# Optimization experiments

Measured on AMD Instinct MI355X. Metric: run time of the kernel, lower is better.

The kernel has to match this reference:

```python
import jax, jax.numpy as jnp
import numpy as np

N_NODES = 50000
N_EDGES = 1_600_000
HID = 64
BN_EPS = 1e-5


def setup_inputs() -> dict:
    key = jax.random.key(0)
    ks = jax.random.split(key, 16)
    x = jax.random.normal(ks[0], (N_NODES, 1), dtype=jnp.float32)
    edge_index = jax.random.randint(ks[1], (2, N_EDGES), 0, N_NODES, dtype=jnp.int32)
    s = 1.0 / np.sqrt(HID)
    # layer 1: 1 -> 64 -> 64
    w1a = jax.random.normal(ks[2], (1, HID), dtype=jnp.float32)
    b1a = jnp.zeros((HID,), jnp.float32)
    w2a = jax.random.normal(ks[3], (HID, HID), dtype=jnp.float32) * s
    b2a = jnp.zeros((HID,), jnp.float32)
    # layers 2-4 stacked: 64 -> 64 -> 64
    w1s = jax.random.normal(ks[4], (3, HID, HID), dtype=jnp.float32) * s
    b1s = jnp.zeros((3, HID), jnp.float32)
    w2s = jax.random.normal(ks[5], (3, HID, HID), dtype=jnp.float32) * s
    b2s = jnp.zeros((3, HID), jnp.float32)
    eps = jnp.zeros((4,), jnp.float32)  # train_eps=True, init 0
    gammas = jnp.ones((4, HID), jnp.float32)
    betas = jnp.zeros((4, HID), jnp.float32)
    fc_w = jax.random.normal(ks[6], (HID, 1), dtype=jnp.float32) * s
    fc_b = jnp.zeros((1,), jnp.float32)
    return {"x": x, "edge_index": edge_index, "w1a": w1a, "b1a": b1a,
            "w2a": w2a, "b2a": b2a, "w1s": w1s, "b1s": b1s, "w2s": w2s,
            "b2s": b2s, "eps": eps, "gammas": gammas, "betas": betas,
            "fc_w": fc_w, "fc_b": fc_b}


def _gin(h, src, dst, e, w1, b1, w2, b2):
    # sum_{j in N(i)} h_j  (messages from src, aggregated at dst)
    agg = jax.ops.segment_sum(h[src], dst, num_segments=N_NODES)
    z = (1.0 + e) * h + agg
    return jax.nn.relu(z @ w1 + b1) @ w2 + b2


def _bn(h, g, b):
    # BatchNorm1d, training mode: biased batch statistics over nodes
    mu = jnp.mean(h, axis=0)
    var = jnp.mean((h - mu) ** 2, axis=0)
    return (h - mu) * jax.lax.rsqrt(var + BN_EPS) * g + b


def reference(x, edge_index, w1a, b1a, w2a, b2a, w1s, b1s, w2s, b2s,
              eps, gammas, betas, fc_w, fc_b):
    src, dst = edge_index[0], edge_index[1]
    h = _bn(jax.nn.relu(_gin(x, src, dst, eps[0], w1a, b1a, w2a, b2a)),
            gammas[0], betas[0])
    for i in range(3):
        h = _bn(jax.nn.relu(_gin(h, src, dst, eps[i + 1],
                                 w1s[i], b1s[i], w2s[i], b2s[i])),
                gammas[i + 1], betas[i + 1])
    return h @ fc_w + fc_b
```

## Files before the change

kernel.cpp:

```cpp
#include <hip/hip_runtime.h>
#include <hip/hip_fp16.h>

#define HID 64
#define BN_EPS 1e-5f
#define WINSH 8
#define WINSZ 256
#define B1 256
#define PIT 72

typedef short bf16x8 __attribute__((ext_vector_type(8)));
typedef float f32x4 __attribute__((ext_vector_type(4)));

__device__ __forceinline__ unsigned short f2b(float f) {
    unsigned int u = __float_as_uint(f);
    u = (u + 0x7FFF + ((u >> 16) & 1)) >> 16;
    return (unsigned short)u;
}
__device__ __forceinline__ float b2f(unsigned short h) {
    return __uint_as_float(((unsigned int)h) << 16);
}
__device__ __forceinline__ f32x4 mfma_bf16(bf16x8 a, bf16x8 b, f32x4 c) {
    return __builtin_amdgcn_mfma_f32_16x16x32_bf16(a, b, c, 0, 0, 0);
}

__global__ __launch_bounds__(256) void prep_kernel(const float* __restrict__ w2a,
                                                   const float* __restrict__ w1s,
                                                   const float* __restrict__ w2s,
                                                   unsigned short* __restrict__ whi,
                                                   unsigned short* __restrict__ wlo,
                                                   float* __restrict__ stats,
                                                   const int* __restrict__ dst,
                                                   int* __restrict__ cnt,
                                                   int E, int nw, int chunk) {
    int blk = blockIdx.x, tid = threadIdx.x;
    if (blk < 7) {
        const float* srcm = (blk == 0) ? w2a : (blk <= 3 ? w1s + (size_t)(blk - 1) * 4096
                                                         : w2s + (size_t)(blk - 4) * 4096);
        unsigned short* dh = whi + (size_t)blk * 4096;
        unsigned short* dl = wlo + (size_t)blk * 4096;
        for (int idx = tid; idx < 4096; idx += 256) {
            int j = idx & 7;
            int lane = (idx >> 3) & 63;
            int ntkh = idx >> 9;
            int nt = ntkh >> 1, kh = ntkh & 1;
            int nc = nt * 16 + (lane & 15);
            int k = kh * 32 + (lane >> 4) * 8 + j;
            float v = srcm[k * 64 + nc];
            unsigned short h = f2b(v);
            dh[idx] = h;
            dl[idx] = f2b(v - b2f(h));
        }
    } else if (blk == 7) {
        stats[tid] = 0.f;
        stats[tid + 256] = 0.f;
    } else {
        __shared__ int c[256];
        int b = blk - 8;
        c[tid] = 0;
        __syncthreads();
        int lo = b * chunk;
        int hi = lo + chunk; if (hi > E) hi = E;
        if ((((size_t)(dst + lo)) & 15) == 0) {
            int n4 = (hi - lo) >> 2;
            const int4* d4p = (const int4*)(dst + lo);
            for (int g = tid; g < n4; g += 256) {
                int4 d4 = d4p[g];
                atomicAdd(&c[d4.x >> WINSH], 1);
                atomicAdd(&c[d4.y >> WINSH], 1);
                atomicAdd(&c[d4.z >> WINSH], 1);
                atomicAdd(&c[d4.w >> WINSH], 1);
            }
            for (int e = lo + (n4 << 2) + tid; e < hi; e += 256)
                atomicAdd(&c[dst[e] >> WINSH], 1);
        } else {
            for (int e = lo + tid; e < hi; e += 256) atomicAdd(&c[dst[e] >> WINSH], 1);
        }
        __syncthreads();
        if (tid < nw) cnt[tid * B1 + b] = c[tid];
    }
}

__global__ __launch_bounds__(256) void scan_a_kernel(const int* __restrict__ in,
                                                     int* __restrict__ partial,
                                                     int* __restrict__ blocksum, int n) {
    __shared__ int sums[256];
    int tid = threadIdx.x;
    int i = blockIdx.x * 256 + tid;
    int v = (i < n) ? in[i] : 0;
    sums[tid] = v;
    __syncthreads();
    for (int off = 1; off < 256; off <<= 1) {
        int t = (tid >= off) ? sums[tid - off] : 0;
        __syncthreads();
        sums[tid] += t;
        __syncthreads();
    }
    if (i < n) partial[i] = sums[tid] - v;
    if (tid == 255) blocksum[blockIdx.x] = sums[255];
}

__global__ __launch_bounds__(256) void p3_bucket_kernel(const int* __restrict__ src,
                                                        const int* __restrict__ dst,
                                                        const int* __restrict__ cpart,
                                                        const int* __restrict__ bsum,
                                                        int* __restrict__ ebuf,
                                                        int E, int nw, int chunk, int nbs2) {
    __shared__ int cur[256];
    __shared__ int sc[256];
    int tid = threadIdx.x, b = blockIdx.x;
    int v = (tid < nbs2) ? bsum[tid] : 0;
    sc[tid] = v;
    __syncthreads();
    for (int off = 1; off < 256; off <<= 1) {
        int t = (tid >= off) ? sc[tid - off] : 0;
        __syncthreads();
        sc[tid] += t;
        __syncthreads();
    }
    int excl = sc[tid] - v;
    if (tid < nw) cur[tid] = cpart[tid * B1 + b] + excl;
    __syncthreads();
    int lo = b * chunk;
    int hi = lo + chunk; if (hi > E) hi = E;
    if (((((size_t)(dst + lo)) | ((size_t)(src + lo))) & 15) == 0) {
        int n4 = (hi - lo) >> 2;
        const int4* d4p = (const int4*)(dst + lo);
        const int4* s4p = (const int4*)(src + lo);
        for (int g = tid; g < n4; g += 256) {
            int4 d4 = d4p[g];
            int4 s4 = s4p[g];
            int p0 = atomicAdd(&cur[d4.x >> WINSH], 1);
            ebuf[p0] = s4.x | ((d4.x & (WINSZ - 1)) << 24);
            int p1 = atomicAdd(&cur[d4.y >> WINSH], 1);
            ebuf[p1] = s4.y | ((d4.y & (WINSZ - 1)) << 24);
            int p2 = atomicAdd(&cur[d4.z >> WINSH], 1);
            ebuf[p2] = s4.z | ((d4.z & (WINSZ - 1)) << 24);
            int p3 = atomicAdd(&cur[d4.w >> WINSH], 1);
            ebuf[p3] = s4.w | ((d4.w & (WINSZ - 1)) << 24);
        }
        for (int e = lo + (n4 << 2) + tid; e < hi; e += 256) {
            int d = dst[e];
            int pos = atomicAdd(&cur[d >> WINSH], 1);
            ebuf[pos] = src[e] | ((d & (WINSZ - 1)) << 24);
        }
    } else {
        for (int e = lo + tid; e < hi; e += 256) {
            int d = dst[e];
            int pos = atomicAdd(&cur[d >> WINSH], 1);
            ebuf[pos] = src[e] | ((d & (WINSZ - 1)) << 24);
        }
    }
}

__global__ __launch_bounds__(256) void p4_fine_kernel(const int* __restrict__ ebuf,
                                                      const int* __restrict__ cpart,
                                                      const int* __restrict__ bsum,
                                                      int* __restrict__ csr_src,
                                                      int* __restrict__ rowptr,
                                                      int* __restrict__ deg,
                                                      int E, int n, int nw, int nbs2) {
    __shared__ int fcnt[256];
    __shared__ int foff[256];
    int tid = threadIdx.x, w = blockIdx.x;
    int bv = (tid < nbs2) ? bsum[tid] : 0;
    foff[tid] = bv;
    __syncthreads();
    for (int off = 1; off < 256; off <<= 1) {
        int t = (tid >= off) ? foff[tid - off] : 0;
        __syncthreads();
        foff[tid] += t;
        __syncthreads();
    }
    int excl = foff[tid] - bv;
    __syncthreads();
    foff[tid] = excl;
    __syncthreads();
    int lo = cpart[w * B1] + foff[w];
    int hi = (w + 1 < nw) ? cpart[(w + 1) * B1] + foff[w + 1] : E;
    __syncthreads();
    fcnt[tid] = 0;
    __syncthreads();
    for (int e = lo + tid; e < hi; e += 256) atomicAdd(&fcnt[(unsigned)ebuf[e] >> 24], 1);
    __syncthreads();
    int v = fcnt[tid];
    foff[tid] = v;
    __syncthreads();
    for (int off = 1; off < 256; off <<= 1) {
        int t = (tid >= off) ? foff[tid - off] : 0;
        __syncthreads();
        foff[tid] += t;
        __syncthreads();
    }
    int myoff = lo + foff[tid] - v;
    int node = w * WINSZ + tid;
    if (node < n) { rowptr[node] = myoff; deg[node] = v; }
    __syncthreads();
    fcnt[tid] = myoff;
    __syncthreads();
    for (int e = lo + tid; e < hi; e += 256) {
        int p = ebuf[e];
        int pos = atomicAdd(&fcnt[(unsigned)p >> 24], 1);
        csr_src[pos] = p & 0xFFFFFF;
    }
}

__global__ __launch_bounds__(256) void gather1_kernel(const float* __restrict__ x,
                                                      const int* __restrict__ rowptr,
                                                      const int* __restrict__ deg,
                                                      const int* __restrict__ csr_src,
                                                      const float* __restrict__ eps,
                                                      float* __restrict__ zscalar, int n) {
    int node = blockIdx.x * 4 + (threadIdx.x >> 6);
    int lane = threadIdx.x & 63;
    if (node >= n) return;
    int start = __builtin_amdgcn_readfirstlane(rowptr[node]);
    int cnt   = __builtin_amdgcn_readfirstlane(deg[node]);
    float a = 0.f;
    for (int i = lane; i < cnt; i += 64) a += x[csr_src[start + i]];
    for (int off = 32; off > 0; off >>= 1) a += __shfl_xor(a, off);
    if (lane == 0) zscalar[node] = (1.0f + eps[0]) * x[node] + a;
}

__global__ __launch_bounds__(256) void gatherz_kernel(const __half* __restrict__ hh16,
                                                      const float* __restrict__ stats_prev,
                                                      const float* __restrict__ gamma_prev,
                                                      const float* __restrict__ beta_prev,
                                                      const int* __restrict__ rowptr,
                                                      const int* __restrict__ deg,
                                                      const int* __restrict__ csr_src,
                                                      const float* __restrict__ eps,
                                                      int layer,
                                                      __half* __restrict__ zh16, int n) {
    int lane = threadIdx.x & 63;
    int half = lane >> 5;
    int fp = lane & 31;
    int node = blockIdx.x * 4 + (threadIdx.x >> 6);

    float inv_n = 1.0f / (float)n;
    float2 sm = ((const float2*)stats_prev)[fp];
    float2 sq = ((const float2*)(stats_prev + 64))[fp];
    float2 gm = ((const float2*)gamma_prev)[fp];
    float2 bt = ((const float2*)beta_prev)[fp];
    float mux = sm.x * inv_n, muy = sm.y * inv_n;
    float scx = gm.x * rsqrtf(sq.x * inv_n - mux * mux + BN_EPS);
    float scy = gm.y * rsqrtf(sq.y * inv_n - muy * muy + BN_EPS);
    float shx = bt.x - mux * scx;
    float shy = bt.y - muy * scy;

    if (node >= n) return;
    int start = __builtin_amdgcn_readfirstlane(rowptr[node]);
    int cnt   = __builtin_amdgcn_readfirstlane(deg[node]);

    const __half2* hh2 = (const __half2*)hh16;
    float ax0 = 0.f, ay0 = 0.f, ax1 = 0.f, ay1 = 0.f;
    float ax2 = 0.f, ay2 = 0.f, ax3 = 0.f, ay3 = 0.f;
    float ax4 = 0.f, ay4 = 0.f, ax5 = 0.f, ay5 = 0.f;
    float ax6 = 0.f, ay6 = 0.f, ax7 = 0.f, ay7 = 0.f;
    int e = 0;
    for (; e + 16 <= cnt; e += 16) {
        int b0  = csr_src[start + e + 0];
        int b1  = csr_src[start + e + 1];
        int b2  = csr_src[start + e + 2];
        int b3  = csr_src[start + e + 3];
        int b4  = csr_src[start + e + 4];
        int b5  = csr_src[start + e + 5];
        int b6  = csr_src[start + e + 6];
        int b7  = csr_src[start + e + 7];
        int b8  = csr_src[start + e + 8];
        int b9  = csr_src[start + e + 9];
        int b10 = csr_src[start + e + 10];
        int b11 = csr_src[start + e + 11];
        int b12 = csr_src[start + e + 12];
        int b13 = csr_src[start + e + 13];
        int b14 = csr_src[start + e + 14];
        int b15 = csr_src[start + e + 15];
        int r0 = half ? b1  : b0;
        int r1 = half ? b3  : b2;
        int r2 = half ? b5  : b4;
        int r3 = half ? b7  : b6;
        int r4 = half ? b9  : b8;
        int r5 = half ? b11 : b10;
        int r6 = half ? b13 : b12;
        int r7 = half ? b15 : b14;
        float2 v0 = __half22float2(hh2[(size_t)r0 * 32 + fp]);
        float2 v1 = __half22float2(hh2[(size_t)r1 * 32 + fp]);
        float2 v2 = __half22float2(hh2[(size_t)r2 * 32 + fp]);
        float2 v3 = __half22float2(hh2[(size_t)r3 * 32 + fp]);
        float2 v4 = __half22float2(hh2[(size_t)r4 * 32 + fp]);
        float2 v5 = __half22float2(hh2[(size_t)r5 * 32 + fp]);
        float2 v6 = __half22float2(hh2[(size_t)r6 * 32 + fp]);
        float2 v7 = __half22float2(hh2[(size_t)r7 * 32 + fp]);
        ax0 += v0.x; ay0 += v0.y;
        ax1 += v1.x; ay1 += v1.y;
        ax2 += v2.x; ay2 += v2.y;
        ax3 += v3.x; ay3 += v3.y;
        ax4 += v4.x; ay4 += v4.y;
        ax5 += v5.x; ay5 += v5.y;
        ax6 += v6.x; ay6 += v6.y;
        ax7 += v7.x; ay7 += v7.y;
    }
    for (; e + 8 <= cnt; e += 8) {
        int s0 = csr_src[start + e + 0];
        int s1 = csr_src[start + e + 1];
        int s2 = csr_src[start + e + 2];
        int s3 = csr_src[start + e + 3];
        int s4 = csr_src[start + e + 4];
        int s5 = csr_src[start + e + 5];
        int s6 = csr_src[start + e + 6];
        int s7 = csr_src[start + e + 7];
        int r0 = half ? s1 : s0;
        int r1 = half ? s3 : s2;
        int r2 = half ? s5 : s4;
        int r3 = half ? s7 : s6;
        float2 v0 = __half22float2(hh2[(size_t)r0 * 32 + fp]);
        float2 v1 = __half22float2(hh2[(size_t)r1 * 32 + fp]);
        float2 v2 = __half22float2(hh2[(size_t)r2 * 32 + fp]);
        float2 v3 = __half22float2(hh2[(size_t)r3 * 32 + fp]);
        ax0 += v0.x; ay0 += v0.y;
        ax1 += v1.x; ay1 += v1.y;
        ax2 += v2.x; ay2 += v2.y;
        ax3 += v3.x; ay3 += v3.y;
    }
    for (; e < cnt; e += 2) {
        int idx = e + half;
        if (idx < cnt) {
            int s = csr_src[start + idx];
            float2 v = __half22float2(hh2[(size_t)s * 32 + fp]);
            ax0 += v.x; ay0 += v.y;
        }
    }
    float sx = ((ax0 + ax1) + (ax2 + ax3)) + ((ax4 + ax5) + (ax6 + ax7));
    float sy = ((ay0 + ay1) + (ay2 + ay3)) + ((ay4 + ay5) + (ay6 + ay7));
    sx += __shfl_xor(sx, 32);
    sy += __shfl_xor(sy, 32);

    float ep = 1.0f + eps[layer];
    float2 self = __half22float2(hh2[(size_t)node * 32 + fp]);
    float zx = fmaf(scx, fmaf(ep, self.x, sx), shx * (ep + (float)cnt));
    float zy = fmaf(scy, fmaf(ep, self.y, sy), shy * (ep + (float)cnt));
    if (half == 0) {
        ((__half2*)zh16)[(size_t)node * 32 + fp] = __floats2half2_rn(zx, zy);
    }
}

__global__ __launch_bounds__(256) void mlp_kernel(const __half* __restrict__ zh16,
                                                  const float* __restrict__ zscalar,
                                                  const float* __restrict__ w1a,
                                                  const float* __restrict__ b1a,
                                                  const unsigned short* __restrict__ w1h,
                                                  const unsigned short* __restrict__ w1l,
                                                  const float* __restrict__ b1v,
                                                  const unsigned short* __restrict__ w2h,
                                                  const unsigned short* __restrict__ w2l,
                                                  const float* __restrict__ b2v,
                                                  float* __restrict__ hpre,
                                                  __half* __restrict__ hh16,
                                                  float* __restrict__ stats,
                                                  int n, int mode,
                                                  int write_hpre, int write_hh) {
    __shared__ __align__(16) unsigned short Ah[64 * PIT];
    __shared__ __align__(16) unsigned short Al[64 * PIT];
    __shared__ float ssum[64], ssq[64];

    int tid = threadIdx.x;
    int base = blockIdx.x * 64;

    if (mode) {
        const unsigned int* z32 = (const unsigned int*)zh16;
        for (int i = tid; i < 2048; i += 256) {
            int nn = i >> 5, c = i & 31;
            unsigned int u = z32[(size_t)(base + nn) * 32 + c];
            __half2 hv = *(__half2*)&u;
            float vx = __half2float(hv.x);
            float vy = __half2float(hv.y);
            unsigned short hx = f2b(vx);
            unsigned short hy = f2b(vy);
            Ah[nn * PIT + 2 * c]     = hx;
            Ah[nn * PIT + 2 * c + 1] = hy;
            Al[nn * PIT + 2 * c]     = f2b(vx - b2f(hx));
            Al[nn * PIT + 2 * c + 1] = f2b(vy - b2f(hy));
        }
    } else {
        for (int i = tid; i < 4096; i += 256) {
            int nn = i >> 6, k = i & 63;
            float zv = zscalar[base + nn];
            float v = fmaxf(fmaf(zv, w1a[k], b1a[k]), 0.f);
            unsigned short h = f2b(v);
            Ah[nn * PIT + k] = h;
            Al[nn * PIT + k] = f2b(v - b2f(h));
        }
    }
    if (tid < 64) { ssum[tid] = 0.f; ssq[tid] = 0.f; }
    __syncthreads();

    int l = tid & 63;
    int m = l & 15;
    int q = l >> 4;
    int m0 = (tid >> 6) * 16;

    const bf16x8* a0h = (const bf16x8*)&Ah[(m0 + m) * PIT + q * 8];
    const bf16x8* a1h = (const bf16x8*)&Ah[(m0 + m) * PIT + 32 + q * 8];
    const bf16x8* a0l = (const bf16x8*)&Al[(m0 + m) * PIT + q * 8];
    const bf16x8* a1l = (const bf16x8*)&Al[(m0 + m) * PIT + 32 + q * 8];

    if (mode) {
        bf16x8 xa0h = *a0h, xa1h = *a1h, xa0l = *a0l, xa1l = *a1l;
        f32x4 acc[4];
#pragma unroll
        for (int nt = 0; nt < 4; ++nt) {
            size_t fo0 = ((size_t)(nt * 2 + 0) * 64 + l) * 8;
            size_t fo1 = ((size_t)(nt * 2 + 1) * 64 + l) * 8;
            bf16x8 b0h = *(const bf16x8*)(w1h + fo0);
            bf16x8 b1h_ = *(const bf16x8*)(w1h + fo1);
            bf16x8 b0l = *(const bf16x8*)(w1l + fo0);
            bf16x8 b1l_ = *(const bf16x8*)(w1l + fo1);
            f32x4 c = {0.f, 0.f, 0.f, 0.f};
            c = mfma_bf16(xa0h, b0h, c);
            c = mfma_bf16(xa0h, b0l, c);
            c = mfma_bf16(xa0l, b0h, c);
            c = mfma_bf16(xa1h, b1h_, c);
            c = mfma_bf16(xa1h, b1l_, c);
            c = mfma_bf16(xa1l, b1h_, c);
            acc[nt] = c;
        }
#pragma unroll
        for (int nt = 0; nt < 4; ++nt) {
            int col = nt * 16 + m;
            float bv = b1v[col];
#pragma unroll
            for (int r = 0; r < 4; ++r) {
                int row = m0 + q * 4 + r;
                float T = fmaxf(acc[nt][r] + bv, 0.f);
                unsigned short h = f2b(T);
                Ah[row * PIT + col] = h;
                Al[row * PIT + col] = f2b(T - b2f(h));
            }
        }
    }
    __syncthreads();

    {
        bf16x8 xa0h = *a0h, xa1h = *a1h, xa0l = *a0l, xa1l = *a1l;
        f32x4 acc[4];
#pragma unroll
        for (int nt = 0; nt < 4; ++nt) {
            size_t fo0 = ((size_t)(nt * 2 + 0) * 64 + l) * 8;
            size_t fo1 = ((size_t)(nt * 2 + 1) * 64 + l) * 8;
            bf16x8 b0h = *(const bf16x8*)(w2h + fo0);
            bf16x8 b1h_ = *(const bf16x8*)(w2h + fo1);
            bf16x8 b0l = *(const bf16x8*)(w2l + fo0);
            bf16x8 b1l_ = *(const bf16x8*)(w2l + fo1);
            f32x4 c = {0.f, 0.f, 0.f, 0.f};
            c = mfma_bf16(xa0h, b0h, c);
            c = mfma_bf16(xa0h, b0l, c);
            c = mfma_bf16(xa0l, b0h, c);
            c = mfma_bf16(xa1h, b1h_, c);
            c = mfma_bf16(xa1h, b1l_, c);
            c = mfma_bf16(xa1l, b1h_, c);
            acc[nt] = c;
        }
#pragma unroll
        for (int nt = 0; nt < 4; ++nt) {
            int col = nt * 16 + m;
            float bv = b2v[col];
            float cs = 0.f, cq = 0.f;
#pragma unroll
            for (int r = 0; r < 4; ++r) {
                int node = base + m0 + q * 4 + r;
                float h = fmaxf(acc[nt][r] + bv, 0.f);
                if (node < n) {
                    if (write_hpre) hpre[(size_t)node * HID + col] = h;
                    if (write_hh) hh16[(size_t)node * HID + col] = __float2half(h);
                    cs += h;
                    cq = fmaf(h, h, cq);
                }
            }
            cs += __shfl_xor(cs, 16); cs += __shfl_xor(cs, 32);
            cq += __shfl_xor(cq, 16); cq += __shfl_xor(cq, 32);
            if (q == 0) {
                atomicAdd(&ssum[col], cs);
                atomicAdd(&ssq[col], cq);
            }
        }
    }
    __syncthreads();
    if (tid < 64) {
        atomicAdd(&stats[tid], ssum[tid]);
        atomicAdd(&stats[64 + tid], ssq[tid]);
    }
}

__global__ __launch_bounds__(256) void final_kernel(const float* __restrict__ hpre,
                                                    const float* __restrict__ stats,
                                                    const float* __restrict__ gamma,
                                                    const float* __restrict__ beta,
                                                    const float* __restrict__ fcw,
                                                    const float* __restrict__ fcb,
                                                    float* __restrict__ out, int n) {
    int wave = threadIdx.x >> 6;
    int lane = threadIdx.x & 63;
    int node = blockIdx.x * 4 + wave;
    if (node < n) {
        float inv_n = 1.0f / (float)n;
        float mu = stats[lane] * inv_n;
        float var = stats[64 + lane] * inv_n - mu * mu;
        float inv = rsqrtf(var + BN_EPS);
        float sc = gamma[lane] * inv;
        float sh = beta[lane] - mu * sc;
        float v = hpre[(size_t)node * HID + lane];
        float t = fmaf(v, sc, sh) * fcw[lane];
        for (int off = 32; off > 0; off >>= 1) t += __shfl_xor(t, off);
        if (lane == 0) out[node] = t + fcb[0];
    }
}

extern "C" void kernel_launch(void* const* d_in, const int* in_sizes, int n_in,
                              void* d_out, int out_size, void* d_ws, size_t ws_size,
                              hipStream_t stream) {
    const float* x      = (const float*)d_in[0];
    const int*   ei     = (const int*)d_in[1];
    const float* w1a    = (const float*)d_in[2];
    const float* b1a    = (const float*)d_in[3];
    const float* w2a    = (const float*)d_in[4];
    const float* b2a    = (const float*)d_in[5];
    const float* w1s    = (const float*)d_in[6];
    const float* b1s    = (const float*)d_in[7];
    const float* w2s    = (const float*)d_in[8];
    const float* b2s    = (const float*)d_in[9];
    const float* eps    = (const float*)d_in[10];
    const float* gammas = (const float*)d_in[11];
    const float* betas  = (const float*)d_in[12];
    const float* fcw    = (const float*)d_in[13];
    const float* fcb    = (const float*)d_in[14];
    float* out = (float*)d_out;

    int n = in_sizes[0];
    int E = in_sizes[1] / 2;
    int npad = ((n + 63) / 64) * 64;
    int nblk = npad / 64;

    int nw = (n + WINSZ - 1) >> WINSH;
    int NWB = nw * B1;
    int chunk = (((E + B1 - 1) / B1) + 3) & ~3;
    int nbs2 = (NWB + 255) / 256;

    const int* src = ei;
    const int* dst = ei + E;

    char* p = (char*)d_ws;
    float* csrtmp  = (float*)p; p += (size_t)npad * HID * 4;
    float* hpre    = (float*)p; p += (size_t)npad * HID * 4;
    __half* hh16   = (__half*)p; p += (size_t)npad * HID * 2;
    __half* zh16   = (__half*)p; p += (size_t)npad * HID * 2;
    float* zscalar = (float*)p; p += (size_t)npad * 4;
    float* stats   = (float*)p; p += 4 * 128 * 4;
    unsigned short* whi = (unsigned short*)p; p += 7 * 4096 * 2;
    unsigned short* wlo = (unsigned short*)p; p += 7 * 4096 * 2;
    int* deg     = (int*)p; p += (size_t)n * 4;
    int* rowptr  = (int*)p; p += (size_t)n * 4;
    int* csr_src = (int*)p; p += (size_t)E * 4;

    int* ebuf     = (int*)csrtmp;
    int* cnt      = ebuf + E;
    int* cpart    = cnt + NWB;
    int* bsum     = cpart + NWB;

    prep_kernel<<<8 + B1, 256, 0, stream>>>(w2a, w1s, w2s, whi, wlo, stats,
                                            dst, cnt, E, nw, chunk);
    scan_a_kernel<<<nbs2, 256, 0, stream>>>(cnt, cpart, bsum, NWB);
    p3_bucket_kernel<<<B1, 256, 0, stream>>>(src, dst, cpart, bsum, ebuf, E, nw, chunk, nbs2);
    p4_fine_kernel<<<nw, 256, 0, stream>>>(ebuf, cpart, bsum, csr_src, rowptr, deg,
                                           E, n, nw, nbs2);

    gather1_kernel<<<(n + 3) / 4, 256, 0, stream>>>(x, rowptr, deg, csr_src, eps, zscalar, n);
    mlp_kernel<<<nblk, 256, 0, stream>>>(zh16, zscalar, w1a, b1a,
                                         whi, wlo, b1a ,
                                         whi , wlo, b2a,
                                         hpre, hh16, stats, n, 0,
                                         0, 1);

    for (int l = 1; l <= 3; ++l) {
        gatherz_kernel<<<(n + 3) / 4, 256, 0, stream>>>(hh16,
                                                        stats + (l - 1) * 128,
                                                        gammas + (l - 1) * HID,
                                                        betas + (l - 1) * HID,
                                                        rowptr, deg, csr_src, eps, l, zh16, n);
        mlp_kernel<<<nblk, 256, 0, stream>>>(zh16, zscalar, w1a, b1a,
                                             whi + (size_t)l * 4096,
                                             wlo + (size_t)l * 4096,
                                             b1s + (size_t)(l - 1) * HID,
                                             whi + (size_t)(3 + l) * 4096,
                                             wlo + (size_t)(3 + l) * 4096,
                                             b2s + (size_t)(l - 1) * HID,
                                             hpre, hh16, stats + l * 128,
                                             n, 1,
                                             (l == 3) ? 1 : 0,
                                             (l < 3) ? 1 : 0);
    }
    final_kernel<<<(n + 3) / 4, 256, 0, stream>>>(hpre, stats + 3 * 128,
                                                  gammas + 3 * HID, betas + 3 * HID,
                                                  fcw, fcb, out, n);
}
```

Baseline: 369.8 us.

## Build CSR with global atomic counting sort and fuse layer-1 gather into scatter

Replaces the two-level windowed bucket sort (shared-memory window counts, bucket scatter, per-window fine sort) with a per-node degree count using global atomics, a scan to rowptr, and a scatter that claims CSR slots via global atomic cursors. The scatter also accumulates x[src] into xsum with float atomics, so the first-layer gather kernel is removed and the MLP computes z directly. This removes kernel launches and the intermediate edge buffer pass, at the cost of heavy contended global atomics over 1.6M edges. Neighbor order within a row and the float sum order become nondeterministic.

```diff
diff --git a/kernel.cpp b/kernel.cpp
--- a/kernel.cpp
+++ b/kernel.cpp
@@ -3,8 +3,6 @@
 
 #define HID 64
 #define BN_EPS 1e-5f
-#define WINSH 8
-#define WINSZ 256
 #define B1 256
 #define PIT 72
 
@@ -21,6 +19,17 @@
 }
 __device__ __forceinline__ f32x4 mfma_bf16(bf16x8 a, bf16x8 b, f32x4 c) {
     return __builtin_amdgcn_mfma_f32_16x16x32_bf16(a, b, c, 0, 0, 0);
+}
+
+__global__ __launch_bounds__(256) void zero_kernel(int* __restrict__ deg,
+                                                   float* __restrict__ xsum,
+                                                   float* __restrict__ stats, int n) {
+    int i = blockIdx.x * 256 + threadIdx.x;
+    if (i < n) { deg[i] = 0; xsum[i] = 0.f; }
+    if (blockIdx.x == 0) {
+        stats[threadIdx.x] = 0.f;
+        stats[threadIdx.x + 256] = 0.f;
+    }
 }
 
 __global__ __launch_bounds__(256) void prep_kernel(const float* __restrict__ w2a,
@@ -28,10 +37,9 @@
                                                    const float* __restrict__ w2s,
                                                    unsigned short* __restrict__ whi,
                                                    unsigned short* __restrict__ wlo,
-                                                   float* __restrict__ stats,
                                                    const int* __restrict__ dst,
-                                                   int* __restrict__ cnt,
-                                                   int E, int nw, int chunk) {
+                                                   int* __restrict__ deg,
+                                                   int E, int chunk) {
     int blk = blockIdx.x, tid = threadIdx.x;
     if (blk < 7) {
         const float* srcm = (blk == 0) ? w2a : (blk <= 3 ? w1s + (size_t)(blk - 1) * 4096
@@ -50,14 +58,8 @@
             dh[idx] = h;
             dl[idx] = f2b(v - b2f(h));
         }
-    } else if (blk == 7) {
-        stats[tid] = 0.f;
-        stats[tid + 256] = 0.f;
     } else {
-        __shared__ int c[256];
-        int b = blk - 8;
-        c[tid] = 0;
-        __syncthreads();
+        int b = blk - 7;
         int lo = b * chunk;
         int hi = lo + chunk; if (hi > E) hi = E;
         if ((((size_t)(dst + lo)) & 15) == 0) {
@@ -65,18 +67,16 @@
             const int4* d4p = (const int4*)(dst + lo);
             for (int g = tid; g < n4; g += 256) {
                 int4 d4 = d4p[g];
-                atomicAdd(&c[d4.x >> WINSH], 1);
-                atomicAdd(&c[d4.y >> WINSH], 1);
-                atomicAdd(&c[d4.z >> WINSH], 1);
-                atomicAdd(&c[d4.w >> WINSH], 1);
+                atomicAdd(&deg[d4.x], 1);
+                atomicAdd(&deg[d4.y], 1);
+                atomicAdd(&deg[d4.z], 1);
+                atomicAdd(&deg[d4.w], 1);
             }
             for (int e = lo + (n4 << 2) + tid; e < hi; e += 256)
-                atomicAdd(&c[dst[e] >> WINSH], 1);
+                atomicAdd(&deg[dst[e]], 1);
         } else {
-            for (int e = lo + tid; e < hi; e += 256) atomicAdd(&c[dst[e] >> WINSH], 1);
-        }
-        __syncthreads();
-        if (tid < nw) cnt[tid * B1 + b] = c[tid];
+            for (int e = lo + tid; e < hi; e += 256) atomicAdd(&deg[dst[e]], 1);
+        }
     }
 }
 
@@ -99,16 +99,15 @@
     if (tid == 255) blocksum[blockIdx.x] = sums[255];
 }
 
-__global__ __launch_bounds__(256) void p3_bucket_kernel(const int* __restrict__ src,
-                                                        const int* __restrict__ dst,
-                                                        const int* __restrict__ cpart,
-                                                        const int* __restrict__ bsum,
-                                                        int* __restrict__ ebuf,
-                                                        int E, int nw, int chunk, int nbs2) {
-    __shared__ int cur[256];
+__global__ __launch_bounds__(256) void finalize_kernel(const int* __restrict__ partial,
+                                                       const int* __restrict__ bsum,
+                                                       int* __restrict__ rowptr,
+                                                       int* __restrict__ cursor,
+                                                       int n, int nbs) {
     __shared__ int sc[256];
-    int tid = threadIdx.x, b = blockIdx.x;
-    int v = (tid < nbs2) ? bsum[tid] : 0;
+    __shared__ int myoff;
+    int tid = threadIdx.x;
+    int v = (tid < nbs) ? bsum[tid] : 0;
     sc[tid] = v;
     __syncthreads();
     for (int off = 1; off < 256; off <<= 1) {
@@ -117,9 +116,24 @@
         sc[tid] += t;
         __syncthreads();
     }
-    int excl = sc[tid] - v;
-    if (tid < nw) cur[tid] = cpart[tid * B1 + b] + excl;
+    if (tid == blockIdx.x) myoff = sc[tid] - v;
     __syncthreads();
+    int i = blockIdx.x * 256 + tid;
+    if (i < n) {
+        int r = partial[i] + myoff;
+        rowptr[i] = r;
+        cursor[i] = r;
+    }
+}
+
+__global__ __launch_bounds__(256) void scatter_kernel(const int* __restrict__ src,
+                                                      const int* __restrict__ dst,
+                                                      const float* __restrict__ x,
+                                                      int* __restrict__ cursor,
+                                                      int* __restrict__ csr_src,
+                                                      float* __restrict__ xsum,
+                                                      int E, int chunk) {
+    int tid = threadIdx.x, b = blockIdx.x;
     int lo = b * chunk;
     int hi = lo + chunk; if (hi > E) hi = E;
     if (((((size_t)(dst + lo)) | ((size_t)(src + lo))) & 15) == 0) {
@@ -129,96 +143,33 @@
         for (int g = tid; g < n4; g += 256) {
             int4 d4 = d4p[g];
             int4 s4 = s4p[g];
-            int p0 = atomicAdd(&cur[d4.x >> WINSH], 1);
-            ebuf[p0] = s4.x | ((d4.x & (WINSZ - 1)) << 24);
-            int p1 = atomicAdd(&cur[d4.y >> WINSH], 1);
-            ebuf[p1] = s4.y | ((d4.y & (WINSZ - 1)) << 24);
-            int p2 = atomicAdd(&cur[d4.z >> WINSH], 1);
-            ebuf[p2] = s4.z | ((d4.z & (WINSZ - 1)) << 24);
-            int p3 = atomicAdd(&cur[d4.w >> WINSH], 1);
-            ebuf[p3] = s4.w | ((d4.w & (WINSZ - 1)) << 24);
+            int p0 = atomicAdd(&cursor[d4.x], 1);
+            csr_src[p0] = s4.x;
+            atomicAdd(&xsum[d4.x], x[s4.x]);
+            int p1 = atomicAdd(&cursor[d4.y], 1);
+            csr_src[p1] = s4.y;
+            atomicAdd(&xsum[d4.y], x[s4.y]);
+            int p2 = atomicAdd(&cursor[d4.z], 1);
+            csr_src[p2] = s4.z;
+            atomicAdd(&xsum[d4.z], x[s4.z]);
+            int p3 = atomicAdd(&cursor[d4.w], 1);
+            csr_src[p3] = s4.w;
+            atomicAdd(&xsum[d4.w], x[s4.w]);
         }
         for (int e = lo + (n4 << 2) + tid; e < hi; e += 256) {
-            int d = dst[e];
-            int pos = atomicAdd(&cur[d >> WINSH], 1);
-            ebuf[pos] = src[e] | ((d & (WINSZ - 1)) << 24);
+            int d = dst[e], s = src[e];
+            int pos = atomicAdd(&cursor[d], 1);
+            csr_src[pos] = s;
+            atomicAdd(&xsum[d], x[s]);
         }
     } else {
         for (int e = lo + tid; e < hi; e += 256) {
-            int d = dst[e];
-            int pos = atomicAdd(&cur[d >> WINSH], 1);
-            ebuf[pos] = src[e] | ((d & (WINSZ - 1)) << 24);
-        }
-    }
-}
-
-__global__ __launch_bounds__(256) void p4_fine_kernel(const int* __restrict__ ebuf,
-                                                      const int* __restrict__ cpart,
-                                                      const int* __restrict__ bsum,
-                                                      int* __restrict__ csr_src,
-                                                      int* __restrict__ rowptr,
-                                                      int* __restrict__ deg,
-                                                      int E, int n, int nw, int nbs2) {
-    __shared__ int fcnt[256];
-    __shared__ int foff[256];
-    int tid = threadIdx.x, w = blockIdx.x;
-    int bv = (tid < nbs2) ? bsum[tid] : 0;
-    foff[tid] = bv;
-    __syncthreads();
-    for (int off = 1; off < 256; off <<= 1) {
-        int t = (tid >= off) ? foff[tid - off] : 0;
-        __syncthreads();
-        foff[tid] += t;
-        __syncthreads();
-    }
-    int excl = foff[tid] - bv;
-    __syncthreads();
-    foff[tid] = excl;
-    __syncthreads();
-    int lo = cpart[w * B1] + foff[w];
-    int hi = (w + 1 < nw) ? cpart[(w + 1) * B1] + foff[w + 1] : E;
-    __syncthreads();
-    fcnt[tid] = 0;
-    __syncthreads();
-    for (int e = lo + tid; e < hi; e += 256) atomicAdd(&fcnt[(unsigned)ebuf[e] >> 24], 1);
-    __syncthreads();
-    int v = fcnt[tid];
-    foff[tid] = v;
-    __syncthreads();
-    for (int off = 1; off < 256; off <<= 1) {
-        int t = (tid >= off) ? foff[tid - off] : 0;
-        __syncthreads();
-        foff[tid] += t;
-        __syncthreads();
-    }
-    int myoff = lo + foff[tid] - v;
-    int node = w * WINSZ + tid;
-    if (node < n) { rowptr[node] = myoff; deg[node] = v; }
-    __syncthreads();
-    fcnt[tid] = myoff;
-    __syncthreads();
-    for (int e = lo + tid; e < hi; e += 256) {
-        int p = ebuf[e];
-        int pos = atomicAdd(&fcnt[(unsigned)p >> 24], 1);
-        csr_src[pos] = p & 0xFFFFFF;
-    }
-}
-
-__global__ __launch_bounds__(256) void gather1_kernel(const float* __restrict__ x,
-                                                      const int* __restrict__ rowptr,
-                                                      const int* __restrict__ deg,
-                                                      const int* __restrict__ csr_src,
-                                                      const float* __restrict__ eps,
-                                                      float* __restrict__ zscalar, int n) {
-    int node = blockIdx.x * 4 + (threadIdx.x >> 6);
-    int lane = threadIdx.x & 63;
-    if (node >= n) return;
-    int start = __builtin_amdgcn_readfirstlane(rowptr[node]);
-    int cnt   = __builtin_amdgcn_readfirstlane(deg[node]);
-    float a = 0.f;
-    for (int i = lane; i < cnt; i += 64) a += x[csr_src[start + i]];
-    for (int off = 32; off > 0; off >>= 1) a += __shfl_xor(a, off);
-    if (lane == 0) zscalar[node] = (1.0f + eps[0]) * x[node] + a;
+            int d = dst[e], s = src[e];
+            int pos = atomicAdd(&cursor[d], 1);
+            csr_src[pos] = s;
+            atomicAdd(&xsum[d], x[s]);
+        }
+    }
 }
 
 __global__ __launch_bounds__(256) void gatherz_kernel(const __half* __restrict__ hh16,
@@ -344,7 +295,9 @@
 }
 
 __global__ __launch_bounds__(256) void mlp_kernel(const __half* __restrict__ zh16,
-                                                  const float* __restrict__ zscalar,
+                                                  const float* __restrict__ x,
+                                                  const float* __restrict__ xsum,
+                                                  const float* __restrict__ eps,
                                                   const float* __restrict__ w1a,
                                                   const float* __restrict__ b1a,
                                                   const unsigned short* __restrict__ w1h,
@@ -381,9 +334,11 @@
             Al[nn * PIT + 2 * c + 1] = f2b(vy - b2f(hy));
         }
     } else {
+        float ep = 1.0f + eps[0];
         for (int i = tid; i < 4096; i += 256) {
             int nn = i >> 6, k = i & 63;
-            float zv = zscalar[base + nn];
+            int node = base + nn;
+            float zv = (node < n) ? fmaf(ep, x[node], xsum[node]) : 0.f;
             float v = fmaxf(fmaf(zv, w1a[k], b1a[k]), 0.f);
             unsigned short h = f2b(v);
             Ah[nn * PIT + k] = h;
@@ -539,10 +494,8 @@
     int npad = ((n + 63) / 64) * 64;
     int nblk = npad / 64;
 
-    int nw = (n + WINSZ - 1) >> WINSH;
-    int NWB = nw * B1;
     int chunk = (((E + B1 - 1) / B1) + 3) & ~3;
-    int nbs2 = (NWB + 255) / 256;
+    int nbs = (n + 255) / 256;
 
     const int* src = ei;
     const int* dst = ei + E;
@@ -552,28 +505,25 @@
     float* hpre    = (float*)p; p += (size_t)npad * HID * 4;
     __half* hh16   = (__half*)p; p += (size_t)npad * HID * 2;
     __half* zh16   = (__half*)p; p += (size_t)npad * HID * 2;
-    float* zscalar = (float*)p; p += (size_t)npad * 4;
+    float* xsum    = (float*)p; p += (size_t)npad * 4;
     float* stats   = (float*)p; p += 4 * 128 * 4;
     unsigned short* whi = (unsigned short*)p; p += 7 * 4096 * 2;
     unsigned short* wlo = (unsigned short*)p; p += 7 * 4096 * 2;
-    int* deg     = (int*)p; p += (size_t)n * 4;
-    int* rowptr  = (int*)p; p += (size_t)n * 4;
+    int* deg     = (int*)p; p += (size_t)npad * 4;
+    int* rowptr  = (int*)p; p += (size_t)npad * 4;
+    int* cursor  = (int*)p; p += (size_t)npad * 4;
     int* csr_src = (int*)p; p += (size_t)E * 4;
 
-    int* ebuf     = (int*)csrtmp;
-    int* cnt      = ebuf + E;
-    int* cpart    = cnt + NWB;
-    int* bsum     = cpart + NWB;
-
-    prep_kernel<<<8 + B1, 256, 0, stream>>>(w2a, w1s, w2s, whi, wlo, stats,
-                                            dst, cnt, E, nw, chunk);
-    scan_a_kernel<<<nbs2, 256, 0, stream>>>(cnt, cpart, bsum, NWB);
-    p3_bucket_kernel<<<B1, 256, 0, stream>>>(src, dst, cpart, bsum, ebuf, E, nw, chunk, nbs2);
-    p4_fine_kernel<<<nw, 256, 0, stream>>>(ebuf, cpart, bsum, csr_src, rowptr, deg,
-                                           E, n, nw, nbs2);
-
-    gather1_kernel<<<(n + 3) / 4, 256, 0, stream>>>(x, rowptr, deg, csr_src, eps, zscalar, n);
-    mlp_kernel<<<nblk, 256, 0, stream>>>(zh16, zscalar, w1a, b1a,
+    int* rp_part = (int*)csrtmp;
+    int* bsum    = rp_part + npad;
+
+    zero_kernel<<<nbs, 256, 0, stream>>>(deg, xsum, stats, n);
+    prep_kernel<<<7 + B1, 256, 0, stream>>>(w2a, w1s, w2s, whi, wlo, dst, deg, E, chunk);
+    scan_a_kernel<<<nbs, 256, 0, stream>>>(deg, rp_part, bsum, n);
+    finalize_kernel<<<nbs, 256, 0, stream>>>(rp_part, bsum, rowptr, cursor, n, nbs);
+    scatter_kernel<<<B1, 256, 0, stream>>>(src, dst, x, cursor, csr_src, xsum, E, chunk);
+
+    mlp_kernel<<<nblk, 256, 0, stream>>>(zh16, x, xsum, eps, w1a, b1a,
                                          whi, wlo, b1a ,
                                          whi , wlo, b2a,
                                          hpre, hh16, stats, n, 0,
@@ -585,7 +535,7 @@
                                                         gammas + (l - 1) * HID,
                                                         betas + (l - 1) * HID,
                                                         rowptr, deg, csr_src, eps, l, zh16, n);
-        mlp_kernel<<<nblk, 256, 0, stream>>>(zh16, zscalar, w1a, b1a,
+        mlp_kernel<<<nblk, 256, 0, stream>>>(zh16, x, xsum, eps, w1a, b1a,
                                              whi + (size_t)l * 4096,
                                              wlo + (size_t)l * 4096,
                                              b1s + (size_t)(l - 1) * HID,
```

Result: slower. 545.1 us (+47.4%).
